# Kernel optimization log

Measured on AMD Instinct MI355X. Metric: run time of the kernel, lower is better.

The kernel has to match this reference:

```python
import jax, jax.numpy as jnp
import numpy as np

N, IN_C, OUT_C = 4096, 256, 64
ALPHA = 0.2  # LeakyReLU negative slope


def setup_inputs() -> dict:
    key = jax.random.key(0)
    k1, k2, k3, k4 = jax.random.split(key, 4)
    H = jax.random.normal(k1, (N, IN_C), dtype=jnp.float32)
    adj = jax.random.randint(k2, (N, N), 0, 2, dtype=jnp.int32)
    # xavier_uniform with gain=1.414
    gain = 1.414
    limW = gain * np.sqrt(6.0 / (IN_C + OUT_C))
    W = jax.random.uniform(k3, (IN_C, OUT_C), minval=-limW, maxval=limW, dtype=jnp.float32)
    lima = gain * np.sqrt(6.0 / (2 * OUT_C + 1))
    a = jax.random.uniform(k4, (2 * OUT_C, 1), minval=-lima, maxval=lima, dtype=jnp.float32)
    return {"H": H, "adj": adj, "W": W, "a": a}


def reference(H, adj, W, a):
    Wh = H @ W  # [N, out_C]
    # Attention_Mat[i,j] = concat(Wh_i, Wh_j); score = Attention_Mat @ a
    # = (Wh @ a1)_i + (Wh @ a2)_j  -- fused, avoids the O(N^2 * 2F) tensor.
    a1, a2 = a[:OUT_C, 0], a[OUT_C:, 0]
    e = (Wh @ a1)[:, None] + (Wh @ a2)[None, :]  # [N, N]
    e = jnp.where(e > 0, e, ALPHA * e)  # LeakyReLU
    att = jax.nn.softmax(e, axis=1)
    # NOTE: original masks AFTER softmax (rows are not renormalized).
    att = jnp.where(adj > 0, att, jnp.zeros_like(att))
    out = att @ Wh  # [N, out_C]
    return jax.nn.elu(out)  # concat=True
```

## Files before the change

### kernel.cpp

```cpp
#include <hip/hip_runtime.h>
#include <math.h>

static constexpr int NN   = 4096;
static constexpr int INC  = 256;
static constexpr int OUTC = 64;

typedef _Float16 half8 __attribute__((ext_vector_type(8)));
typedef float floatx4 __attribute__((ext_vector_type(4)));

__device__ __forceinline__ float lrelu(float x) {
    return fmaxf(x, 0.f) + 0.2f * fminf(x, 0.f);
}
__device__ __forceinline__ float elu1(float x) {
    return x > 0.f ? x : (__expf(x) - 1.f);
}

__global__ __launch_bounds__(256) void k_pack(const int* __restrict__ adj,
                                              unsigned int* __restrict__ bits) {
    const int tau = blockIdx.x * 256 + threadIdx.x;
    const int4* src = (const int4*)adj + (size_t)tau * 8;
    unsigned int out = 0;
    #pragma unroll
    for (int u = 0; u < 8; ++u) {
        const int4 v = src[u];
        const unsigned int nib = (unsigned int)(v.x > 0)
                               | ((unsigned int)(v.y > 0) << 1)
                               | ((unsigned int)(v.z > 0) << 2)
                               | ((unsigned int)(v.w > 0) << 3);
        out |= nib << (4 * u);
    }
    bits[tau] = out;
}

__global__ __launch_bounds__(256) void k_wh(const float* __restrict__ H,
                                            const float* __restrict__ W,
                                            const float* __restrict__ a,
                                            unsigned short* __restrict__ WhT,
                                            float* __restrict__ f1,
                                            float* __restrict__ f2) {
    __shared__ __align__(16) float Wl[INC * OUTC];
    __shared__ __align__(16) float Hl[16 * INC];
    __shared__ _Float16 Tl[16 * 68];
    const int t = threadIdx.x;
    const int i0 = blockIdx.x * 16;
    {
        const float4* W4 = (const float4*)W;
        float4* Wl4 = (float4*)Wl;
        #pragma unroll
        for (int u = 0; u < 16; ++u) Wl4[u * 256 + t] = W4[u * 256 + t];
        const float4* H4 = (const float4*)(H + i0 * INC);
        float4* Hl4 = (float4*)Hl;
        #pragma unroll
        for (int u = 0; u < 4; ++u) Hl4[u * 256 + t] = H4[u * 256 + t];
    }
    __syncthreads();
    const int c = t & 63;
    const int g = t >> 6;
    const float a1c = a[c];
    const float a2c = a[OUTC + c];
    float acc[4] = {0.f, 0.f, 0.f, 0.f};
    const float4* Hl4 = (const float4*)Hl;
    for (int k4 = 0; k4 < INC / 4; ++k4) {
        const float w0 = Wl[(k4 * 4 + 0) * OUTC + c];
        const float w1 = Wl[(k4 * 4 + 1) * OUTC + c];
        const float w2 = Wl[(k4 * 4 + 2) * OUTC + c];
        const float w3 = Wl[(k4 * 4 + 3) * OUTC + c];
        #pragma unroll
        for (int s = 0; s < 4; ++s) {
            const float4 h = Hl4[(g + 4 * s) * (INC / 4) + k4];
            acc[s] = fmaf(h.x, w0, fmaf(h.y, w1, fmaf(h.z, w2, fmaf(h.w, w3, acc[s]))));
        }
    }
    #pragma unroll
    for (int s = 0; s < 4; ++s) {
        const int r = g + 4 * s;
        Tl[r * 68 + c] = (_Float16)acc[s];
        float v1 = acc[s] * a1c;
        float v2 = acc[s] * a2c;
        #pragma unroll
        for (int off = 32; off; off >>= 1) {
            v1 += __shfl_xor(v1, off);
            v2 += __shfl_xor(v2, off);
        }
        if (c == 0) { f1[i0 + r] = v1; f2[i0 + r] = v2; }
    }
    __syncthreads();
    const int c2 = t >> 2;
    const int rs = (t & 3) * 4;
    ushort4 u;
    u.x = *(const unsigned short*)&Tl[(rs + 0) * 68 + c2];
    u.y = *(const unsigned short*)&Tl[(rs + 1) * 68 + c2];
    u.z = *(const unsigned short*)&Tl[(rs + 2) * 68 + c2];
    u.w = *(const unsigned short*)&Tl[(rs + 3) * 68 + c2];
    *(ushort4*)(WhT + c2 * NN + i0 + rs) = u;
}

__global__ __launch_bounds__(1024, 4) void k_att(const unsigned char* __restrict__ bits,
                                                 const _Float16* __restrict__ WhT,
                                                 const float* __restrict__ f1,
                                                 const float* __restrict__ f2,
                                                 float* __restrict__ out) {
    __shared__ __align__(16) float sf2[NN];
    __shared__ __align__(16) float sacc[16 * 1024];
    __shared__ float sden[16 * 16];
    __shared__ float smax[16];
    const int t = threadIdx.x;
    const int w = t >> 6;
    const int l = t & 63;
    const int m = l & 15;
    const int quad = l >> 4;
    const int i0 = blockIdx.x * 16;

    {
        const float4 v = ((const float4*)f2)[t];
        ((float4*)sf2)[t] = v;
        float mloc = fmaxf(fmaxf(v.x, v.y), fmaxf(v.z, v.w));
        #pragma unroll
        for (int off = 32; off; off >>= 1) mloc = fmaxf(mloc, __shfl_xor(mloc, off));
        if (l == 0) smax[w] = mloc;
    }
    __syncthreads();
    float maxf2 = smax[0];
    #pragma unroll
    for (int k = 1; k < 16; ++k) maxf2 = fmaxf(maxf2, smax[k]);

    const float f1r = f1[i0 + m];
    const float mrow = lrelu(f1r + maxf2);
    float den = 0.f;
    floatx4 acc[4] = {{0.f,0.f,0.f,0.f},{0.f,0.f,0.f,0.f},{0.f,0.f,0.f,0.f},{0.f,0.f,0.f,0.f}};
    const int jbase = w * 32 + quad * 8;
    const unsigned char* brow = bits + (size_t)(i0 + m) * (NN / 8) + (jbase >> 3);
    unsigned int m8[8];
    #pragma unroll
    for (int it = 0; it < 8; ++it) m8[it] = brow[it * 64];

    #pragma unroll 2
    for (int it = 0; it < 8; ++it) {
        const int j = jbase + it * 512;
        const unsigned int mb = m8[it];
        const float4 g0 = *(const float4*)(sf2 + j);
        const float4 g1 = *(const float4*)(sf2 + j + 4);
        half8 af;
        {
            float p;
            p = __expf(lrelu(f1r + g0.x) - mrow); den += p; af[0] = (mb & 1u)   ? (_Float16)p : (_Float16)0.f;
            p = __expf(lrelu(f1r + g0.y) - mrow); den += p; af[1] = (mb & 2u)   ? (_Float16)p : (_Float16)0.f;
            p = __expf(lrelu(f1r + g0.z) - mrow); den += p; af[2] = (mb & 4u)   ? (_Float16)p : (_Float16)0.f;
            p = __expf(lrelu(f1r + g0.w) - mrow); den += p; af[3] = (mb & 8u)   ? (_Float16)p : (_Float16)0.f;
            p = __expf(lrelu(f1r + g1.x) - mrow); den += p; af[4] = (mb & 16u)  ? (_Float16)p : (_Float16)0.f;
            p = __expf(lrelu(f1r + g1.y) - mrow); den += p; af[5] = (mb & 32u)  ? (_Float16)p : (_Float16)0.f;
            p = __expf(lrelu(f1r + g1.z) - mrow); den += p; af[6] = (mb & 64u)  ? (_Float16)p : (_Float16)0.f;
            p = __expf(lrelu(f1r + g1.w) - mrow); den += p; af[7] = (mb & 128u) ? (_Float16)p : (_Float16)0.f;
        }
        #pragma unroll
        for (int nt = 0; nt < 4; ++nt) {
            const half8 bf = *(const half8*)(WhT + (size_t)(nt * 16 + m) * NN + j);
            acc[nt] = __builtin_amdgcn_mfma_f32_16x16x32_f16(af, bf, acc[nt], 0, 0, 0);
        }
    }
    den += __shfl_xor(den, 16);
    den += __shfl_xor(den, 32);
    if (l < 16) sden[w * 16 + l] = den;
    #pragma unroll
    for (int nt = 0; nt < 4; ++nt)
        #pragma unroll
        for (int r = 0; r < 4; ++r)
            sacc[w * 1024 + (quad * 4 + r) * 64 + nt * 16 + m] = acc[nt][r];
    __syncthreads();
    float s = 0.f;
    #pragma unroll
    for (int w2 = 0; w2 < 16; ++w2) s += sacc[w2 * 1024 + t];
    float dden = 0.f;
    const int row = t >> 6;
    #pragma unroll
    for (int w2 = 0; w2 < 16; ++w2) dden += sden[w2 * 16 + row];
    out[(size_t)i0 * OUTC + t] = elu1(s / dden);
}

extern "C" void kernel_launch(void* const* d_in, const int* in_sizes, int n_in,
                              void* d_out, int out_size, void* d_ws, size_t ws_size,
                              hipStream_t stream) {
    const float* H  = (const float*)d_in[0];
    const int* adj  = (const int*)d_in[1];
    const float* W  = (const float*)d_in[2];
    const float* a  = (const float*)d_in[3];
    float* out = (float*)d_out;
    char* ws = (char*)d_ws;
    unsigned short* WhT = (unsigned short*)(ws);
    float* f1 = (float*)(ws + (512 << 10));
    float* f2 = (float*)(ws + (528 << 10));
    unsigned int* bits = (unsigned int*)(ws + (1 << 20));
    hipLaunchKernelGGL(k_pack, dim3(2048), dim3(256), 0, stream, adj, bits);
    hipLaunchKernelGGL(k_wh,   dim3(256),  dim3(256), 0, stream, H, W, a, WhT, f1, f2);
    hipLaunchKernelGGL(k_att,  dim3(256),  dim3(1024), 0, stream,
                       (const unsigned char*)bits, (const _Float16*)WhT, f1, f2, out);
}
```

Before: 129.2 us.

## Merge adjacency packing and Wh projection into one prep kernel, read W from global

Combines the adjacency bit-packing kernel and the Wh/f1/f2 projection kernel into a single launch. Blocks 0-255 do the projection and the rest do packing, so the two run concurrently and one launch disappears. The projection blocks no longer stage the 64 KB W matrix in LDS and instead read it directly from global/cache with a partially unrolled loop. This cuts LDS footprint and staging time and raises occupancy, at the cost of repeated global/L2 reads of W per block.

```diff
diff --git a/kernel.cpp b/kernel.cpp
--- a/kernel.cpp
+++ b/kernel.cpp
@@ -15,39 +15,35 @@
     return x > 0.f ? x : (__expf(x) - 1.f);
 }
 
-__global__ __launch_bounds__(256) void k_pack(const int* __restrict__ adj,
-                                              unsigned int* __restrict__ bits) {
-    const int tau = blockIdx.x * 256 + threadIdx.x;
-    const int4* src = (const int4*)adj + (size_t)tau * 8;
-    unsigned int out = 0;
-    #pragma unroll
-    for (int u = 0; u < 8; ++u) {
-        const int4 v = src[u];
-        const unsigned int nib = (unsigned int)(v.x > 0)
-                               | ((unsigned int)(v.y > 0) << 1)
-                               | ((unsigned int)(v.z > 0) << 2)
-                               | ((unsigned int)(v.w > 0) << 3);
-        out |= nib << (4 * u);
+__global__ __launch_bounds__(256) void k_prep(const int* __restrict__ adj,
+                                              unsigned int* __restrict__ bits,
+                                              const float* __restrict__ H,
+                                              const float* __restrict__ W,
+                                              const float* __restrict__ a,
+                                              unsigned short* __restrict__ WhT,
+                                              float* __restrict__ f1,
+                                              float* __restrict__ f2) {
+    const int t = threadIdx.x;
+    if (blockIdx.x >= 256) {
+        const int tau = (blockIdx.x - 256) * 256 + t;
+        const int4* src = (const int4*)adj + (size_t)tau * 8;
+        unsigned int o = 0;
+        #pragma unroll
+        for (int u = 0; u < 8; ++u) {
+            const int4 v = src[u];
+            const unsigned int nib = (unsigned int)(v.x > 0)
+                                   | ((unsigned int)(v.y > 0) << 1)
+                                   | ((unsigned int)(v.z > 0) << 2)
+                                   | ((unsigned int)(v.w > 0) << 3);
+            o |= nib << (4 * u);
+        }
+        bits[tau] = o;
+        return;
     }
-    bits[tau] = out;
-}
-
-__global__ __launch_bounds__(256) void k_wh(const float* __restrict__ H,
-                                            const float* __restrict__ W,
-                                            const float* __restrict__ a,
-                                            unsigned short* __restrict__ WhT,
-                                            float* __restrict__ f1,
-                                            float* __restrict__ f2) {
-    __shared__ __align__(16) float Wl[INC * OUTC];
     __shared__ __align__(16) float Hl[16 * INC];
     __shared__ _Float16 Tl[16 * 68];
-    const int t = threadIdx.x;
     const int i0 = blockIdx.x * 16;
     {
-        const float4* W4 = (const float4*)W;
-        float4* Wl4 = (float4*)Wl;
-        #pragma unroll
-        for (int u = 0; u < 16; ++u) Wl4[u * 256 + t] = W4[u * 256 + t];
         const float4* H4 = (const float4*)(H + i0 * INC);
         float4* Hl4 = (float4*)Hl;
         #pragma unroll
@@ -60,11 +56,12 @@
     const float a2c = a[OUTC + c];
     float acc[4] = {0.f, 0.f, 0.f, 0.f};
     const float4* Hl4 = (const float4*)Hl;
+    #pragma unroll 4
     for (int k4 = 0; k4 < INC / 4; ++k4) {
-        const float w0 = Wl[(k4 * 4 + 0) * OUTC + c];
-        const float w1 = Wl[(k4 * 4 + 1) * OUTC + c];
-        const float w2 = Wl[(k4 * 4 + 2) * OUTC + c];
-        const float w3 = Wl[(k4 * 4 + 3) * OUTC + c];
+        const float w0 = W[(k4 * 4 + 0) * OUTC + c];
+        const float w1 = W[(k4 * 4 + 1) * OUTC + c];
+        const float w2 = W[(k4 * 4 + 2) * OUTC + c];
+        const float w3 = W[(k4 * 4 + 3) * OUTC + c];
         #pragma unroll
         for (int s = 0; s < 4; ++s) {
             const float4 h = Hl4[(g + 4 * s) * (INC / 4) + k4];
@@ -190,8 +187,8 @@
     float* f1 = (float*)(ws + (512 << 10));
     float* f2 = (float*)(ws + (528 << 10));
     unsigned int* bits = (unsigned int*)(ws + (1 << 20));
-    hipLaunchKernelGGL(k_pack, dim3(2048), dim3(256), 0, stream, adj, bits);
-    hipLaunchKernelGGL(k_wh,   dim3(256),  dim3(256), 0, stream, H, W, a, WhT, f1, f2);
+    hipLaunchKernelGGL(k_prep, dim3(2304), dim3(256), 0, stream,
+                       adj, bits, H, W, a, WhT, f1, f2);
     hipLaunchKernelGGL(k_att,  dim3(256),  dim3(1024), 0, stream,
                        (const unsigned char*)bits, (const _Float16*)WhT, f1, f2, out);
 }
```

Measured after the change: 123.5 us (median of 2 runs). 1.05x faster.
